# Performance work log

Hardware: AMD Instinct MI355X
Metric: run time of the kernel (lower is better)

Reference implementation:

```python
import jax, jax.numpy as jnp
import numpy as np

N, E, DIN, H, HEADS = 50000, 800000, 128, 64, 4


def setup_inputs() -> dict:
    key = jax.random.key(0)
    ks = jax.random.split(key, 12)

    def p(k, shape, fan_in):
        return jax.random.normal(k, shape, dtype=jnp.float32) / np.float32(np.sqrt(fan_in))

    return dict(
        x=jax.random.normal(ks[0], (N, DIN), dtype=jnp.float32),
        edge_index=jax.random.randint(ks[1], (2, E), 0, N, dtype=jnp.int32),
        # GCNConv(input_dim, hidden)
        W_gcn=p(ks[2], (DIN, H), DIN), b_gcn=jnp.zeros((H,), jnp.float32),
        # GATConv(hidden, hidden, heads=4, concat=True)
        W_gat=p(ks[3], (H, HEADS * H), H),
        att_src=p(ks[4], (HEADS, H), H), att_dst=p(ks[5], (HEADS, H), H),
        b_gat=jnp.zeros((HEADS * H,), jnp.float32),
        # SAGEConv(4*hidden, hidden): lin_l (neighbors, with bias), lin_r (root, no bias)
        W_sage_l=p(ks[6], (HEADS * H, H), HEADS * H), b_sage=jnp.zeros((H,), jnp.float32),
        W_sage_r=p(ks[7], (HEADS * H, H), HEADS * H),
        # edge-pair MLP: Linear(2*hidden, hidden) -> ReLU -> Linear(hidden, 1)
        W1=p(ks[8], (2 * H, H), 2 * H), b1=jnp.zeros((H,), jnp.float32),
        W2=p(ks[9], (H, 1), H), b2=jnp.zeros((1,), jnp.float32),
    )


def reference(x, edge_index, W_gcn, b_gcn, W_gat, att_src, att_dst, b_gat,
              W_sage_l, b_sage, W_sage_r, W1, b1, W2, b2):
    n = x.shape[0]
    src, dst = edge_index[0], edge_index[1]
    loop = jnp.arange(n, dtype=edge_index.dtype)
    # edges with self-loops appended (GCN and GAT add self-loops by default)
    s2 = jnp.concatenate([src, loop])
    d2 = jnp.concatenate([dst, loop])

    h = x @ W_gcn                                            # [N, H]
    deg = jax.ops.segment_sum(jnp.ones_like(d2, jnp.float32), d2, num_segments=n)
    dinv = jnp.where(deg > 0, jax.lax.rsqrt(jnp.maximum(deg, 1e-12)), 0.0)
    norm = dinv[s2] * dinv[d2]                               # [E+N]
    h = jax.ops.segment_sum(h[s2] * norm[:, None], d2, num_segments=n) + b_gcn
    h = jax.nn.relu(h)                                       # dropout: identity in eval

    # ---- GATConv (heads=4, concat=True, negative_slope=0.2) ----
    g = (h @ W_gat).reshape(n, HEADS, H)                     # [N, heads, C]
    a_s = jnp.sum(g * att_src, axis=-1)                      # [N, heads]
    a_d = jnp.sum(g * att_dst, axis=-1)
    e = jax.nn.leaky_relu(a_s[s2] + a_d[d2], 0.2)            # [E+N, heads]
    m = jax.ops.segment_max(e, d2, num_segments=n)           # per-target max (stable softmax)
    e = jnp.exp(e - m[d2])
    z = jax.ops.segment_sum(e, d2, num_segments=n)
    alpha = e / (z[d2] + 1e-16)                              # edge softmax over incoming edges
    g = jax.ops.segment_sum(g[s2] * alpha[:, :, None], d2, num_segments=n)
    g = jax.nn.relu(g.reshape(n, HEADS * H) + b_gat)

    # ---- SAGEConv (mean aggregation, root weight, no self-loops) ----
    nsum = jax.ops.segment_sum(g[src], dst, num_segments=n)
    cnt = jax.ops.segment_sum(jnp.ones_like(dst, jnp.float32), dst, num_segments=n)
    mean = nsum / jnp.maximum(cnt, 1.0)[:, None]
    s = jax.nn.relu(mean @ W_sage_l + b_sage + g @ W_sage_r)  # [N, H]

    # ---- edge-pair MLP + sigmoid ----
    ef = jnp.concatenate([s[src], s[dst]], axis=1)            # [E, 2H]
    pred = jax.nn.relu(ef @ W1 + b1) @ W2 + b2                # [E, 1]
    return jax.nn.sigmoid(pred[:, 0])
```

## Files before the change

### kernel.cpp

```cpp
#include <hip/hip_runtime.h>
#include <math.h>

typedef float v2f __attribute__((ext_vector_type(2)));
static __device__ __forceinline__ float4 f4s(float v){ return make_float4(v,v,v,v); }
static __device__ __forceinline__ float4 f4add(float4 a, float4 b){ return make_float4(a.x+b.x,a.y+b.y,a.z+b.z,a.w+b.w); }
static __device__ __forceinline__ float4 f4max(float4 a, float4 b){ return make_float4(fmaxf(a.x,b.x),fmaxf(a.y,b.y),fmaxf(a.z,b.z),fmaxf(a.w,b.w)); }
static __device__ __forceinline__ float4 f4scale(float4 a, float s){ return make_float4(a.x*s,a.y*s,a.z*s,a.w*s); }
static __device__ __forceinline__ float4 f4fma(float4 acc, float s, float4 b){
  acc.x += s*b.x; acc.y += s*b.y; acc.z += s*b.z; acc.w += s*b.w; return acc;
}
static __device__ __forceinline__ float4 f4relu(float4 a){ return f4max(a, f4s(0.f)); }
static __device__ __forceinline__ float4 f4leaky(float4 a){
  return make_float4(a.x>0.f?a.x:0.2f*a.x, a.y>0.f?a.y:0.2f*a.y, a.z>0.f?a.z:0.2f*a.z, a.w>0.f?a.w:0.2f*a.w);
}
static __device__ __forceinline__ float4 f4expf(float4 a){ return make_float4(__expf(a.x),__expf(a.y),__expf(a.z),__expf(a.w)); }
static __device__ __forceinline__ unsigned short f2bf(float f){
  unsigned int u = __float_as_uint(f);
  unsigned int r = (u + 0x7fffu + ((u >> 16) & 1u)) >> 16;
  return (unsigned short)r;
}
static __device__ __forceinline__ ushort4 f2bf4(float4 f){
  ushort4 r; r.x=f2bf(f.x); r.y=f2bf(f.y); r.z=f2bf(f.z); r.w=f2bf(f.w); return r;
}
static __device__ __forceinline__ float4 bfu2f4(uint2 u){
  return make_float4(__uint_as_float(u.x << 16), __uint_as_float(u.x & 0xffff0000u),
                     __uint_as_float(u.y << 16), __uint_as_float(u.y & 0xffff0000u));
}
static __device__ __forceinline__ float4 bfu2f4_lo(uint4 u){ return bfu2f4(make_uint2(u.x, u.y)); }
static __device__ __forceinline__ float4 bfu2f4_hi(uint4 u){ return bfu2f4(make_uint2(u.z, u.w)); }

typedef __attribute__((ext_vector_type(8))) unsigned short u16x8;
static __device__ __forceinline__ u16x8 f2bf8(float4 a, float4 b){
  u16x8 r;
  r[0]=f2bf(a.x); r[1]=f2bf(a.y); r[2]=f2bf(a.z); r[3]=f2bf(a.w);
  r[4]=f2bf(b.x); r[5]=f2bf(b.y); r[6]=f2bf(b.z); r[7]=f2bf(b.w);
  return r;
}
static __device__ __forceinline__ void red2(float4& a, float4& b){
  a.x += __shfl_xor(a.x, 8); a.y += __shfl_xor(a.y, 8);
  a.z += __shfl_xor(a.z, 8); a.w += __shfl_xor(a.w, 8);
  b.x += __shfl_xor(b.x, 8); b.y += __shfl_xor(b.y, 8);
  b.z += __shfl_xor(b.z, 8); b.w += __shfl_xor(b.w, 8);
}
static __device__ __forceinline__ unsigned char f2fp8(float v){
  return (unsigned char)(__builtin_amdgcn_cvt_pk_fp8_f32(v, v, 0, false) & 0xff);
}
static __device__ __forceinline__ unsigned int f4_fp8x4(float4 v){
  unsigned int r = __builtin_amdgcn_cvt_pk_fp8_f32(v.x, v.y, 0, false);
  r = __builtin_amdgcn_cvt_pk_fp8_f32(v.z, v.w, r, true);
  return r;
}
static __device__ __forceinline__ float4 fp8x4_f4(unsigned int q){
  v2f lo = __builtin_amdgcn_cvt_pk_f32_fp8(q, false);
  v2f hi = __builtin_amdgcn_cvt_pk_f32_fp8(q, true);
  return make_float4(lo[0], lo[1], hi[0], hi[1]);
}
static __device__ __forceinline__ float dot8(float4 a, float4 b, const float* v){
  return a.x*v[0]+a.y*v[1]+a.z*v[2]+a.w*v[3]+b.x*v[4]+b.y*v[5]+b.z*v[6]+b.w*v[7];
}

typedef __attribute__((ext_vector_type(8))) short bf16x8;
typedef __attribute__((ext_vector_type(4))) float f32x4;

__global__ __launch_bounds__(256) void k_rank(const int* __restrict__ dst, int* __restrict__ cnt,
                                              int* __restrict__ rank, int E){
  int t = blockIdx.x*256 + threadIdx.x;
  if (t < E) rank[t] = atomicAdd(&cnt[dst[t]], 1);
}
__global__ __launch_bounds__(256) void k_scan1(const int* __restrict__ cnt, int* __restrict__ excl,
                                               int* __restrict__ bsum, int n){
  __shared__ int sc[256];
  int t = threadIdx.x; int i = blockIdx.x*256 + t;
  int v = (i<n)?cnt[i]:0;
  sc[t]=v; __syncthreads();
  for (int o=1;o<256;o<<=1){ int a=(t>=o)?sc[t-o]:0; __syncthreads(); sc[t]+=a; __syncthreads(); }
  if (i<n) excl[i] = sc[t]-v;
  if (t==255) bsum[blockIdx.x] = sc[t];
}
__global__ __launch_bounds__(256) void k_scan2v(int* __restrict__ bsum, int nb,
                                                const float* __restrict__ Wg, const float* __restrict__ as,
                                                const float* __restrict__ ad, float* __restrict__ Vs,
                                                float* __restrict__ Vd){
  __shared__ int sc[256];
  int t = threadIdx.x;
  int v = (t<nb)?bsum[t]:0;
  sc[t]=v; __syncthreads();
  for (int o=1;o<256;o<<=1){ int a=(t>=o)?sc[t-o]:0; __syncthreads(); sc[t]+=a; __syncthreads(); }
  if (t<nb) bsum[t] = sc[t]-v;
  int h = t >> 6, k = t & 63;
  float s = 0.f, d = 0.f;
  const float* wr = Wg + (size_t)k*256 + h*64;
  const float* ar = as + h*64;
  const float* dr = ad + h*64;
  for (int c = 0; c < 64; ++c){ float w = wr[c]; s += w*ar[c]; d += w*dr[c]; }
  Vs[t] = s; Vd[t] = d;
}
__global__ __launch_bounds__(256) void k_scan3(const int* __restrict__ cnt, const int* __restrict__ excl,
                                               const int* __restrict__ bsum, int* __restrict__ offs,
                                               float* __restrict__ dinv, int n, int E){
  int i = blockIdx.x*256 + threadIdx.x;
  if (i < n){
    int o = excl[i] + bsum[blockIdx.x];
    offs[i] = o;
    dinv[i] = rsqrtf((float)cnt[i] + 1.0f);
    if (i == 0) offs[n] = E;
  }
}
__global__ __launch_bounds__(256) void k_fill(const int* __restrict__ src, const int* __restrict__ dst,
                                              const int* __restrict__ offs, const int* __restrict__ rank,
                                              int* __restrict__ csr, int E){
  int t = blockIdx.x*256 + threadIdx.x;
  if (t < E) csr[offs[dst[t]] + rank[t]] = src[t];
}

template<int K, int Cout, bool IBF16, bool SCALE, bool DUAL, bool H4, bool BRELU, bool OB16, bool O8>
__global__ __launch_bounds__(256) void k_mgemm(const void* __restrict__ in, int ldin,
                                               const float* __restrict__ Wa, int ldwa,
                                               const float* __restrict__ Wb, int ldwb,
                                               unsigned short* __restrict__ out,
                                               unsigned char* __restrict__ out8, int ldout,
                                               int n, const float* __restrict__ rowscale,
                                               const float* __restrict__ bias){
  constexpr int CC = Cout >> 4;
  constexpr int KB = K >> 5;
  constexpr int NH = H4 ? 4 : 1;
  extern __shared__ unsigned short wb[];
  int tid = threadIdx.x;
  constexpr int nslots = KB*CC*64;
  for (int s = tid; s < nslots; s += 256){
    int l = s & 63;
    int f = s >> 6;
    int cc = f % CC, kb = f / CC;
    int c  = cc*16 + (l & 15);
    int kr = kb*32 + ((l >> 4) << 3);
    const float* wp; int ld;
    if (DUAL && c >= (Cout/2)){ wp = Wb + (size_t)kr*ldwb + (c - Cout/2); ld = ldwb; }
    else                      { wp = Wa + (size_t)kr*ldwa + c;            ld = ldwa; }
    unsigned short* dp = &wb[s*8];
    #pragma unroll
    for (int j = 0; j < 8; ++j) dp[j] = f2bf(wp[(size_t)j*ld]);
  }
  __syncthreads();
  int wv = tid >> 6, l = tid & 63;
  int lrow = l & 15;
  int lk = (l >> 4) << 3;
  int ngrp = (n + 63) >> 6;
  const unsigned short* inb = (const unsigned short*)in;
  const float* inf = (const float*)in;
  for (int g = blockIdx.x; g < ngrp; g += gridDim.x){
    int r0 = (g << 6) + (wv << 4);
    int m = r0 + lrow;
    bf16x8 afr[NH][KB];
    #pragma unroll
    for (int h = 0; h < NH; ++h){
      #pragma unroll
      for (int kb = 0; kb < KB; ++kb){
        bf16x8 a = {0,0,0,0,0,0,0,0};
        if (m < n){
          int off = (H4 ? h*64 : 0) + kb*32 + lk;
          if (IBF16){
            a = *(const bf16x8*)(inb + (size_t)m*ldin + off);
          } else {
            const float* p = inf + (size_t)m*ldin + off;
            float4 f0 = *(const float4*)p;
            float4 f1 = *(const float4*)(p + 4);
            a[0]=(short)f2bf(f0.x); a[1]=(short)f2bf(f0.y); a[2]=(short)f2bf(f0.z); a[3]=(short)f2bf(f0.w);
            a[4]=(short)f2bf(f1.x); a[5]=(short)f2bf(f1.y); a[6]=(short)f2bf(f1.z); a[7]=(short)f2bf(f1.w);
          }
        }
        afr[h][kb] = a;
      }
    }
    int rbase = r0 + ((l >> 4) << 2);
    float sc[4];
    if (SCALE){
      #pragma unroll
      for (int r = 0; r < 4; ++r) sc[r] = (rbase + r < n) ? rowscale[rbase + r] : 0.f;
    }
    #pragma unroll
    for (int cc = 0; cc < CC; ++cc){
      f32x4 acc = {0.f, 0.f, 0.f, 0.f};
      constexpr int hstep = H4 ? 1 : 0;
      int hh = hstep ? (cc >> 2) : 0;
      #pragma unroll
      for (int kb = 0; kb < KB; ++kb){
        bf16x8 b = *(const bf16x8*)&wb[((kb*CC + cc)*64 + l)*8];
        acc = __builtin_amdgcn_mfma_f32_16x16x32_bf16(afr[hh][kb], b, acc, 0, 0, 0);
      }
      int c = cc*16 + lrow;
      float bv = BRELU ? bias[c] : 0.f;
      #pragma unroll
      for (int r = 0; r < 4; ++r){
        int rr = rbase + r;
        if (rr < n){
          float v = acc[r];
          if (SCALE) v *= sc[r];
          if (BRELU) v = fmaxf(v + bv, 0.f);
          if (OB16) out[(size_t)rr*ldout + c] = f2bf(v);
          if (O8)   out8[(size_t)rr*ldout + c] = f2fp8(v);
        }
      }
    }
  }
}

__global__ __launch_bounds__(256) void k_gatsage(const unsigned short* __restrict__ Y,
                                                 const float* __restrict__ Wg,
                                                 const float* __restrict__ bg,
                                                 const float* __restrict__ Wl,
                                                 const float* __restrict__ Wr,
                                                 unsigned short* __restrict__ R,
                                                 unsigned char* __restrict__ P8, int n){
  constexpr int LDG = 264;
  extern __shared__ unsigned short lds[];
  unsigned short* wb1 = lds;
  unsigned short* wb2 = wb1 + 2048*8;
  unsigned short* gb  = wb2 + 4096*8;
  int tid = threadIdx.x;
  for (int s = tid; s < 2048; s += 256){
    int l = s & 63, f = s >> 6;
    int cc = f & 15, kb = f >> 4;
    int c  = cc*16 + (l & 15);
    int kr = kb*32 + ((l >> 4) << 3);
    const float* wp = Wg + (size_t)kr*256 + c;
    unsigned short* dp = &wb1[s*8];
    #pragma unroll
    for (int j = 0; j < 8; ++j) dp[j] = f2bf(wp[(size_t)j*256]);
  }
  for (int s = tid; s < 4096; s += 256){
    int l = s & 63, f = s >> 6;
    int cc = f & 7, kb = f >> 3;
    int c  = cc*16 + (l & 15);
    int kr = kb*32 + ((l >> 4) << 3);
    const float* wp = (c >= 64) ? (Wr + (size_t)kr*64 + (c - 64)) : (Wl + (size_t)kr*64 + c);
    unsigned short* dp = &wb2[s*8];
    #pragma unroll
    for (int j = 0; j < 8; ++j) dp[j] = f2bf(wp[(size_t)j*64]);
  }
  __syncthreads();
  int wv = tid >> 6, l = tid & 63;
  int lrow = l & 15;
  int lk = (l >> 4) << 3;
  int rbase4 = (l >> 4) << 2;
  int ngrp = (n + 63) >> 6;
  for (int g = blockIdx.x; g < ngrp; g += gridDim.x){
    int r0 = (g << 6) + (wv << 4);
    int m = r0 + lrow;
    bf16x8 afr[4][2];
    #pragma unroll
    for (int h = 0; h < 4; ++h){
      #pragma unroll
      for (int kb = 0; kb < 2; ++kb){
        bf16x8 a = {0,0,0,0,0,0,0,0};
        if (m < n) a = *(const bf16x8*)(Y + (size_t)m*256 + h*64 + kb*32 + lk);
        afr[h][kb] = a;
      }
    }
    #pragma unroll
    for (int cc = 0; cc < 16; ++cc){
      f32x4 acc = {0.f, 0.f, 0.f, 0.f};
      int hh = cc >> 2;
      #pragma unroll
      for (int kb = 0; kb < 2; ++kb){
        bf16x8 b = *(const bf16x8*)&wb1[((kb*16 + cc)*64 + l)*8];
        acc = __builtin_amdgcn_mfma_f32_16x16x32_bf16(afr[hh][kb], b, acc, 0, 0, 0);
      }
      int c = cc*16 + lrow;
      float bv = bg[c];
      #pragma unroll
      for (int r = 0; r < 4; ++r){
        int lr = (wv << 4) + rbase4 + r;
        gb[lr*LDG + c] = f2bf(fmaxf(acc[r] + bv, 0.f));
      }
    }
    bf16x8 afb[8];
    #pragma unroll
    for (int kb = 0; kb < 8; ++kb)
      afb[kb] = *(const bf16x8*)&gb[((wv << 4) + lrow)*LDG + kb*32 + lk];
    #pragma unroll
    for (int cc = 0; cc < 8; ++cc){
      f32x4 acc = {0.f, 0.f, 0.f, 0.f};
      #pragma unroll
      for (int kb = 0; kb < 8; ++kb){
        bf16x8 b = *(const bf16x8*)&wb2[((kb*8 + cc)*64 + l)*8];
        acc = __builtin_amdgcn_mfma_f32_16x16x32_bf16(afb[kb], b, acc, 0, 0, 0);
      }
      int c = cc*16 + lrow;
      #pragma unroll
      for (int r = 0; r < 4; ++r){
        int rr = r0 + rbase4 + r;
        if (rr < n){
          float v = acc[r];
          if (c < 64) P8[(size_t)rr*64 + c] = f2fp8(v);
          else        R[(size_t)rr*64 + (c - 64)] = f2bf(v);
        }
      }
    }
  }
}

__global__ __launch_bounds__(256) void k_gcn(const unsigned char* __restrict__ a8, const float* __restrict__ dinv,
                                             const float* __restrict__ b, const int* __restrict__ offs,
                                             const int* __restrict__ csr, const float* __restrict__ Vs,
                                             const float* __restrict__ Vd, unsigned char* __restrict__ h8,
                                             float* __restrict__ D, int n){
  __shared__ float svs[256], svd[256];
  svs[threadIdx.x] = Vs[threadIdx.x];
  svd[threadIdx.x] = Vd[threadIdx.x];
  __syncthreads();
  int l = threadIdx.x & 63;
  int node = (((blockIdx.x*256 + threadIdx.x) >> 6) << 2) + (l >> 4);
  int l15 = l & 15;
  int grp = l15 >> 3, sub = l15 & 7;
  bool ok = node < n;
  int beg = 0, end = 0;
  float di = 0.f;
  if (ok){ beg = offs[node]; end = offs[node+1]; di = dinv[node]; }
  float4 aL0 = f4s(0.f), aH0 = f4s(0.f), aL1 = f4s(0.f), aH1 = f4s(0.f);
  int i = beg + grp;
  for (; i + 2 < end; i += 4){
    int s0 = csr[i], s1 = csr[i+2];
    uint2 u0 = *(const uint2*)(a8 + (size_t)s0*64 + (sub<<3));
    uint2 u1 = *(const uint2*)(a8 + (size_t)s1*64 + (sub<<3));
    aL0 = f4add(aL0, fp8x4_f4(u0.x)); aH0 = f4add(aH0, fp8x4_f4(u0.y));
    aL1 = f4add(aL1, fp8x4_f4(u1.x)); aH1 = f4add(aH1, fp8x4_f4(u1.y));
  }
  if (i < end){
    int s0 = csr[i];
    uint2 u0 = *(const uint2*)(a8 + (size_t)s0*64 + (sub<<3));
    aL0 = f4add(aL0, fp8x4_f4(u0.x)); aH0 = f4add(aH0, fp8x4_f4(u0.y));
  }
  float4 aL = f4add(aL0, aL1), aH = f4add(aH0, aH1);
  red2(aL, aH);
  if (ok){
    uint2 us = *(const uint2*)(a8 + (size_t)node*64 + (sub<<3));
    aL = f4add(aL, fp8x4_f4(us.x)); aH = f4add(aH, fp8x4_f4(us.y));
    float4 b0 = *(const float4*)(b + (sub<<3));
    float4 b1 = *(const float4*)(b + (sub<<3) + 4);
    float4 r0 = f4relu(f4fma(b0, di, aL));
    float4 r1 = f4relu(f4fma(b1, di, aH));
    if (grp == 0){
      uint2 q; q.x = f4_fp8x4(r0); q.y = f4_fp8x4(r1);
      *(uint2*)(h8 + (size_t)node*64 + (sub<<3)) = q;
    }
    const float* vs0 = svs + (grp*128) + (sub<<3);
    const float* vd0 = svd + (grp*128) + (sub<<3);
    float s0 = dot8(r0, r1, vs0);
    float s1 = dot8(r0, r1, vs0 + 64);
    float d0 = dot8(r0, r1, vd0);
    float d1 = dot8(r0, r1, vd0 + 64);
    #pragma unroll
    for (int o = 1; o < 8; o <<= 1){
      s0 += __shfl_xor(s0, o); s1 += __shfl_xor(s1, o);
      d0 += __shfl_xor(d0, o); d1 += __shfl_xor(d1, o);
    }
    if (sub == 0){
      *(float2*)(D + (size_t)node*8 + grp*2)     = make_float2(s0, s1);
      *(float2*)(D + (size_t)node*8 + 4 + grp*2) = make_float2(d0, d1);
    }
  }
}

#define GAT_CAP 128
__global__ __launch_bounds__(256) void k_gat2(const float* __restrict__ D, const unsigned char* __restrict__ H8,
                                              const int* __restrict__ offs, const int* __restrict__ csr,
                                              unsigned short* __restrict__ Y, int n){
  __shared__ float wl[8][GAT_CAP*4];
  __shared__ int   sl[8][GAT_CAP];
  int hw = threadIdx.x >> 5;
  int node = (blockIdx.x*256 + threadIdx.x) >> 5;
  int l5 = threadIdx.x & 31;
  if (node >= n) return;
  int beg = offs[node], end = offs[node+1];
  int deg = end - beg;
  float4 ed  = *(const float4*)(D + (size_t)node*8 + 4);
  float4 es0 = *(const float4*)(D + (size_t)node*8);
  float4 wself = f4expf(f4leaky(f4add(es0, ed)));
  float4 z4 = f4s(0.f);
  for (int i = beg + l5; i < end; i += 32){
    int s = csr[i];
    float4 w = f4expf(f4leaky(f4add(*(const float4*)(D + (size_t)s*8), ed)));
    int li = i - beg;
    if (li < GAT_CAP){ *(float4*)&wl[hw][li<<2] = w; sl[hw][li] = s << 6; }
    z4 = f4add(z4, w);
  }
  for (int m = 1; m < 32; m <<= 1){
    z4.x += __shfl_xor(z4.x, m); z4.y += __shfl_xor(z4.y, m);
    z4.z += __shfl_xor(z4.z, m); z4.w += __shfl_xor(z4.w, m);
  }
  z4 = f4add(z4, wself);
  int grp = l5 >> 4;
  int sub = l5 & 15;
  int c0b = sub << 2;
  float4 a0 = f4s(0.f), a1 = f4s(0.f), a2 = f4s(0.f), a3 = f4s(0.f);
  int nl = deg < GAT_CAP ? deg : GAT_CAP;
  int i = grp;
  for (; i + 2 < nl; i += 4){
    int o0 = sl[hw][i], o1 = sl[hw][i+2];
    float4 w0 = *(const float4*)&wl[hw][i<<2];
    float4 w1 = *(const float4*)&wl[hw][(i+2)<<2];
    unsigned int q0 = *(const unsigned int*)(H8 + o0 + c0b);
    unsigned int q1 = *(const unsigned int*)(H8 + o1 + c0b);
    float4 f0 = fp8x4_f4(q0);
    float4 f1 = fp8x4_f4(q1);
    a0 = f4fma(a0, w0.x, f0); a1 = f4fma(a1, w0.y, f0);
    a2 = f4fma(a2, w0.z, f0); a3 = f4fma(a3, w0.w, f0);
    a0 = f4fma(a0, w1.x, f1); a1 = f4fma(a1, w1.y, f1);
    a2 = f4fma(a2, w1.z, f1); a3 = f4fma(a3, w1.w, f1);
  }
  if (i < nl){
    float4 w0 = *(const float4*)&wl[hw][i<<2];
    float4 f0 = fp8x4_f4(*(const unsigned int*)(H8 + sl[hw][i] + c0b));
    a0 = f4fma(a0, w0.x, f0); a1 = f4fma(a1, w0.y, f0);
    a2 = f4fma(a2, w0.z, f0); a3 = f4fma(a3, w0.w, f0);
  }
  for (int j = nl + grp; j < deg; j += 2){
    int s = csr[beg+j];
    float4 e = f4leaky(f4add(*(const float4*)(D + (size_t)s*8), ed));
    float4 w = f4expf(e);
    float4 f0 = fp8x4_f4(*(const unsigned int*)(H8 + ((size_t)s << 6) + c0b));
    a0 = f4fma(a0, w.x, f0); a1 = f4fma(a1, w.y, f0);
    a2 = f4fma(a2, w.z, f0); a3 = f4fma(a3, w.w, f0);
  }
  a0.x += __shfl_xor(a0.x, 16); a0.y += __shfl_xor(a0.y, 16); a0.z += __shfl_xor(a0.z, 16); a0.w += __shfl_xor(a0.w, 16);
  a1.x += __shfl_xor(a1.x, 16); a1.y += __shfl_xor(a1.y, 16); a1.z += __shfl_xor(a1.z, 16); a1.w += __shfl_xor(a1.w, 16);
  a2.x += __shfl_xor(a2.x, 16); a2.y += __shfl_xor(a2.y, 16); a2.z += __shfl_xor(a2.z, 16); a2.w += __shfl_xor(a2.w, 16);
  a3.x += __shfl_xor(a3.x, 16); a3.y += __shfl_xor(a3.y, 16); a3.z += __shfl_xor(a3.z, 16); a3.w += __shfl_xor(a3.w, 16);
  if (grp == 0){
    float4 fs = fp8x4_f4(*(const unsigned int*)(H8 + ((size_t)node << 6) + c0b));
    a0 = f4fma(a0, wself.x, fs);
    a1 = f4fma(a1, wself.y, fs);
    a2 = f4fma(a2, wself.z, fs);
    a3 = f4fma(a3, wself.w, fs);
    a0 = f4scale(a0, 1.f/(z4.x + 1e-16f));
    a1 = f4scale(a1, 1.f/(z4.y + 1e-16f));
    a2 = f4scale(a2, 1.f/(z4.z + 1e-16f));
    a3 = f4scale(a3, 1.f/(z4.w + 1e-16f));
    unsigned short* yp = Y + (size_t)node*256 + (sub << 2);
    *(ushort4*)(yp)       = f2bf4(a0);
    *(ushort4*)(yp + 64)  = f2bf4(a1);
    *(ushort4*)(yp + 128) = f2bf4(a2);
    *(ushort4*)(yp + 192) = f2bf4(a3);
  }
}

__global__ __launch_bounds__(256) void k_sage(const unsigned char* __restrict__ P8, const unsigned short* __restrict__ R,
                                              const float* __restrict__ b, const int* __restrict__ offs,
                                              const int* __restrict__ csr, const float* __restrict__ W1a,
                                              const float* __restrict__ W1b, unsigned char* __restrict__ T2, int n){
  __shared__ unsigned short wfr[1024*8];
  __shared__ unsigned short stile[16][72];
  int tid = threadIdx.x;
  for (int s = tid; s < 1024; s += 256){
    int l = s & 63, f = s >> 6;
    int cc = f & 7, kb = f >> 3;
    int c  = cc*16 + (l & 15);
    int kr = kb*32 + ((l >> 4) << 3);
    const float* wp = (c >= 64) ? (W1b + (size_t)kr*64 + (c - 64)) : (W1a + (size_t)kr*64 + c);
    unsigned short* dp = &wfr[s*8];
    #pragma unroll
    for (int j = 0; j < 8; ++j) dp[j] = f2bf(wp[(size_t)j*64]);
  }
  int wv = tid >> 6, l = tid & 63;
  int base = blockIdx.x*16;
  int lrow16 = (wv << 2) + (l >> 4);
  int node = base + lrow16;
  int l15 = l & 15;
  int grp = l15 >> 3, sub = l15 & 7;
  bool ok = node < n;
  int beg = 0, end = 0;
  if (ok){ beg = offs[node]; end = offs[node+1]; }
  float4 aL0 = f4s(0.f), aH0 = f4s(0.f), aL1 = f4s(0.f), aH1 = f4s(0.f);
  int i = beg + grp;
  for (; i + 2 < end; i += 4){
    int s0 = csr[i], s1 = csr[i+2];
    uint2 u0 = *(const uint2*)(P8 + (size_t)s0*64 + (sub<<3));
    uint2 u1 = *(const uint2*)(P8 + (size_t)s1*64 + (sub<<3));
    aL0 = f4add(aL0, fp8x4_f4(u0.x)); aH0 = f4add(aH0, fp8x4_f4(u0.y));
    aL1 = f4add(aL1, fp8x4_f4(u1.x)); aH1 = f4add(aH1, fp8x4_f4(u1.y));
  }
  if (i < end){
    int s0 = csr[i];
    uint2 u0 = *(const uint2*)(P8 + (size_t)s0*64 + (sub<<3));
    aL0 = f4add(aL0, fp8x4_f4(u0.x)); aH0 = f4add(aH0, fp8x4_f4(u0.y));
  }
  float4 aL = f4add(aL0, aL1), aH = f4add(aH0, aH1);
  red2(aL, aH);
  float4 r0 = f4s(0.f), r1 = f4s(0.f);
  if (ok){
    float minv = 1.f / fmaxf((float)(end - beg), 1.f);
    uint4 ur = *(const uint4*)(R + (size_t)node*64 + (sub<<3));
    float4 b0 = *(const float4*)(b + (sub<<3));
    float4 b1 = *(const float4*)(b + (sub<<3) + 4);
    r0 = f4relu(f4add(f4fma(b0, minv, aL), bfu2f4_lo(ur)));
    r1 = f4relu(f4add(f4fma(b1, minv, aH), bfu2f4_hi(ur)));
  }
  if (grp == 0) *(u16x8*)&stile[lrow16][sub << 3] = f2bf8(r0, r1);
  __syncthreads();
  int lrow = l & 15, lk = (l >> 4) << 3;
  bf16x8 af0 = *(const bf16x8*)&stile[lrow][lk];
  bf16x8 af1 = *(const bf16x8*)&stile[lrow][32 + lk];
  int rbase = (l >> 4) << 2;
  #pragma unroll
  for (int q = 0; q < 2; ++q){
    int cc = wv*2 + q;
    f32x4 acc = {0.f, 0.f, 0.f, 0.f};
    acc = __builtin_amdgcn_mfma_f32_16x16x32_bf16(af0, *(const bf16x8*)&wfr[(cc*64 + l)*8], acc, 0, 0, 0);
    acc = __builtin_amdgcn_mfma_f32_16x16x32_bf16(af1, *(const bf16x8*)&wfr[((8 + cc)*64 + l)*8], acc, 0, 0, 0);
    int c = cc*16 + lrow;
    #pragma unroll
    for (int r = 0; r < 4; ++r){
      int nd = base + rbase + r;
      if (nd < n) T2[(size_t)nd*128 + c] = f2fp8(acc[r]);
    }
  }
}

__global__ __launch_bounds__(256) void k_mlp(const unsigned char* __restrict__ T2,
                                             const float* __restrict__ b1, const float* __restrict__ W2,
                                             const float* __restrict__ b2, const int* __restrict__ src,
                                             const int* __restrict__ dst, float* __restrict__ out, int E){
  int t = threadIdx.x;
  int e = blockIdx.x*32 + (t >> 3);
  if (e >= E) return;
  int sub = t & 7;
  int s = src[e], d = dst[e];
  uint2 uu = *(const uint2*)(T2 + (size_t)s*128 + (sub<<3));
  uint2 vv = *(const uint2*)(T2 + (size_t)d*128 + 64 + (sub<<3));
  float4 u0 = fp8x4_f4(uu.x), u1 = fp8x4_f4(uu.y);
  float4 v0 = fp8x4_f4(vv.x), v1 = fp8x4_f4(vv.y);
  float4 bb0 = *(const float4*)(b1 + (sub<<3));
  float4 bb1 = *(const float4*)(b1 + (sub<<3) + 4);
  float4 w0 = *(const float4*)(W2 + (sub<<3));
  float4 w1 = *(const float4*)(W2 + (sub<<3) + 4);
  float4 ta = f4relu(f4add(f4add(u0, v0), bb0));
  float4 tb = f4relu(f4add(f4add(u1, v1), bb1));
  float p = ta.x*w0.x + ta.y*w0.y + ta.z*w0.z + ta.w*w0.w
          + tb.x*w1.x + tb.y*w1.y + tb.z*w1.z + tb.w*w1.w;
  p += __shfl_xor(p, 1);
  p += __shfl_xor(p, 2);
  p += __shfl_xor(p, 4);
  if (sub == 0) out[e] = 1.f / (1.f + __expf(-(p + b2[0])));
}

extern "C" void kernel_launch(void* const* d_in, const int* in_sizes, int n_in,
                              void* d_out, int out_size, void* d_ws, size_t ws_size,
                              hipStream_t stream){
  const float* x     = (const float*)d_in[0];
  const int*   eidx  = (const int*)  d_in[1];
  const float* W_gcn = (const float*)d_in[2];
  const float* b_gcn = (const float*)d_in[3];
  const float* W_gat = (const float*)d_in[4];
  const float* att_s = (const float*)d_in[5];
  const float* att_d = (const float*)d_in[6];
  const float* b_gat = (const float*)d_in[7];
  const float* W_sl  = (const float*)d_in[8];
  const float* b_sg  = (const float*)d_in[9];
  const float* W_sr  = (const float*)d_in[10];
  const float* W1    = (const float*)d_in[11];
  const float* b1    = (const float*)d_in[12];
  const float* W2    = (const float*)d_in[13];
  const float* b2    = (const float*)d_in[14];
  float* out = (float*)d_out;

  const int N = in_sizes[0] / 128;
  const int E = in_sizes[1] / 2;
  const int* src = eidx;
  const int* dst = eidx + E;

  float* ws   = (float*)d_ws;
  float* dinv = ws;
  float* D    = dinv + (size_t)N;
  float* Vs   = D + (size_t)N*8;
  float* Vd   = Vs + 256;
  unsigned short* Y  = (unsigned short*)(Vd + 256);
  unsigned short* R  = Y + (size_t)N*256;
  unsigned char*  A8 = (unsigned char*)(R + (size_t)N*64);
  unsigned char*  H8 = A8 + (size_t)N*64;
  unsigned char*  P8 = H8 + (size_t)N*64;
  unsigned char*  T2 = P8 + (size_t)N*64;
  int* cnt  = (int*)(T2 + (size_t)N*128);
  int* excl = cnt + N;
  int* bsum = excl + N;
  int* offs = bsum + 256;
  int* rank = offs + N + 1;
  int* csr  = rank + E;

  const int nb = (N + 255) / 256;
  const int gtiles = (N + 63) / 64;
  const int nwb = (N + 15) / 16;
  const int GSH = (2048*8 + 4096*8 + 64*264) * 2;

  static bool s_attr = false;
  if (!s_attr){
    hipFuncSetAttribute((const void*)k_gatsage, hipFuncAttributeMaxDynamicSharedMemorySize, GSH);
    s_attr = true;
  }

  hipMemsetAsync(cnt, 0, (size_t)N*sizeof(int), stream);
  k_rank<<<(E+255)/256, 256, 0, stream>>>(dst, cnt, rank, E);
  k_scan1<<<nb, 256, 0, stream>>>(cnt, excl, bsum, N);
  k_scan2v<<<1, 256, 0, stream>>>(bsum, nb, W_gat, att_s, att_d, Vs, Vd);
  k_scan3<<<nb, 256, 0, stream>>>(cnt, excl, bsum, offs, dinv, N, E);
  k_fill<<<(E+255)/256, 256, 0, stream>>>(src, dst, offs, rank, csr, E);

  k_mgemm<128, 64, false, true, false, false, false, false, true><<<gtiles, 256, 128*64*2, stream>>>(
      x, 128, W_gcn, 64, nullptr, 0, nullptr, A8, 64, N, dinv, nullptr);
  k_gcn <<<nwb, 256, 0, stream>>>(A8, dinv, b_gcn, offs, csr, Vs, Vd, H8, D, N);

  k_gat2<<<(N+7)/8, 256, 0, stream>>>(D, H8, offs, csr, Y, N);

  k_gatsage<<<256, 256, GSH, stream>>>(Y, W_gat, b_gat, W_sl, W_sr, R, P8, N);

  k_sage<<<nwb, 256, 0, stream>>>(P8, R, b_sg, offs, csr, W1, W1 + 64*64, T2, N);

  k_mlp <<<(E+31)/32, 256, 0, stream>>>(T2, b1, W2, b2, src, dst, out, E);
}
```

Before: 290.5 us.

## Merge preprocessing kernels to cut launches: fold scan2 into scan1/scan3, fuse fill with GCN GEMM

Moves the attention-vector precomputation into an extra block of the first scan kernel. Each block of the third scan now redoes the block-sum scan itself, which removes the single-block second scan launch. The CSR fill and the GCN input GEMM (x·W_gcn scaled by dinv, written as fp8) share one launch, with block ranges assigned to each job. This cuts the launch count from seven to four and lets the GEMM overlap the irregular scatter, at the cost of redundant block-sum scans and a specialized, non-persistent GEMM.

New measurement: 285.6 us. Within noise of the previous version (-1.7%).

```diff
diff --git a/kernel.cpp b/kernel.cpp
--- a/kernel.cpp
+++ b/kernel.cpp
@@ -67,8 +67,22 @@
   int t = blockIdx.x*256 + threadIdx.x;
   if (t < E) rank[t] = atomicAdd(&cnt[dst[t]], 1);
 }
-__global__ __launch_bounds__(256) void k_scan1(const int* __restrict__ cnt, int* __restrict__ excl,
-                                               int* __restrict__ bsum, int n){
+__global__ __launch_bounds__(256) void k_scan1v(const int* __restrict__ cnt, int* __restrict__ excl,
+                                                int* __restrict__ bsum, int n, int nb,
+                                                const float* __restrict__ Wg, const float* __restrict__ as,
+                                                const float* __restrict__ ad, float* __restrict__ Vs,
+                                                float* __restrict__ Vd){
+  if ((int)blockIdx.x == nb){
+    int t = threadIdx.x;
+    int h = t >> 6, k = t & 63;
+    float s = 0.f, d = 0.f;
+    const float* wr = Wg + (size_t)k*256 + h*64;
+    const float* ar = as + h*64;
+    const float* dr = ad + h*64;
+    for (int c = 0; c < 64; ++c){ float w = wr[c]; s += w*ar[c]; d += w*dr[c]; }
+    Vs[t] = s; Vd[t] = d;
+    return;
+  }
   __shared__ int sc[256];
   int t = threadIdx.x; int i = blockIdx.x*256 + t;
   int v = (i<n)?cnt[i]:0;
@@ -77,129 +91,83 @@
   if (i<n) excl[i] = sc[t]-v;
   if (t==255) bsum[blockIdx.x] = sc[t];
 }
-__global__ __launch_bounds__(256) void k_scan2v(int* __restrict__ bsum, int nb,
-                                                const float* __restrict__ Wg, const float* __restrict__ as,
-                                                const float* __restrict__ ad, float* __restrict__ Vs,
-                                                float* __restrict__ Vd){
-  __shared__ int sc[256];
+__global__ __launch_bounds__(256) void k_scan3b(const int* __restrict__ cnt, const int* __restrict__ excl,
+                                                const int* __restrict__ bsum, int* __restrict__ offs,
+                                                float* __restrict__ dinv, int n, int E, int nb){
+  __shared__ int sb[256];
   int t = threadIdx.x;
   int v = (t<nb)?bsum[t]:0;
-  sc[t]=v; __syncthreads();
-  for (int o=1;o<256;o<<=1){ int a=(t>=o)?sc[t-o]:0; __syncthreads(); sc[t]+=a; __syncthreads(); }
-  if (t<nb) bsum[t] = sc[t]-v;
-  int h = t >> 6, k = t & 63;
-  float s = 0.f, d = 0.f;
-  const float* wr = Wg + (size_t)k*256 + h*64;
-  const float* ar = as + h*64;
-  const float* dr = ad + h*64;
-  for (int c = 0; c < 64; ++c){ float w = wr[c]; s += w*ar[c]; d += w*dr[c]; }
-  Vs[t] = s; Vd[t] = d;
-}
-__global__ __launch_bounds__(256) void k_scan3(const int* __restrict__ cnt, const int* __restrict__ excl,
-                                               const int* __restrict__ bsum, int* __restrict__ offs,
-                                               float* __restrict__ dinv, int n, int E){
-  int i = blockIdx.x*256 + threadIdx.x;
+  sb[t]=v; __syncthreads();
+  for (int o=1;o<256;o<<=1){ int a=(t>=o)?sb[t-o]:0; __syncthreads(); sb[t]+=a; __syncthreads(); }
+  int bex = sb[blockIdx.x] - bsum[blockIdx.x];
+  int i = blockIdx.x*256 + t;
   if (i < n){
-    int o = excl[i] + bsum[blockIdx.x];
-    offs[i] = o;
+    offs[i] = excl[i] + bex;
     dinv[i] = rsqrtf((float)cnt[i] + 1.0f);
     if (i == 0) offs[n] = E;
   }
 }
-__global__ __launch_bounds__(256) void k_fill(const int* __restrict__ src, const int* __restrict__ dst,
-                                              const int* __restrict__ offs, const int* __restrict__ rank,
-                                              int* __restrict__ csr, int E){
-  int t = blockIdx.x*256 + threadIdx.x;
-  if (t < E) csr[offs[dst[t]] + rank[t]] = src[t];
-}
-
-template<int K, int Cout, bool IBF16, bool SCALE, bool DUAL, bool H4, bool BRELU, bool OB16, bool O8>
-__global__ __launch_bounds__(256) void k_mgemm(const void* __restrict__ in, int ldin,
-                                               const float* __restrict__ Wa, int ldwa,
-                                               const float* __restrict__ Wb, int ldwb,
-                                               unsigned short* __restrict__ out,
-                                               unsigned char* __restrict__ out8, int ldout,
-                                               int n, const float* __restrict__ rowscale,
-                                               const float* __restrict__ bias){
-  constexpr int CC = Cout >> 4;
-  constexpr int KB = K >> 5;
-  constexpr int NH = H4 ? 4 : 1;
-  extern __shared__ unsigned short wb[];
+
+__global__ __launch_bounds__(256) void k_fillg(const int* __restrict__ src, const int* __restrict__ dstv,
+                                               const int* __restrict__ offs, const int* __restrict__ rank,
+                                               int* __restrict__ csr, int E, int fb,
+                                               const float* __restrict__ x, const float* __restrict__ Wg,
+                                               unsigned char* __restrict__ a8, int n,
+                                               const float* __restrict__ dinv){
+  if ((int)blockIdx.x < fb){
+    int t = blockIdx.x*256 + threadIdx.x;
+    if (t < E) csr[offs[dstv[t]] + rank[t]] = src[t];
+    return;
+  }
+  __shared__ unsigned short wb[1024*8];
   int tid = threadIdx.x;
-  constexpr int nslots = KB*CC*64;
-  for (int s = tid; s < nslots; s += 256){
-    int l = s & 63;
-    int f = s >> 6;
-    int cc = f % CC, kb = f / CC;
+  for (int s = tid; s < 1024; s += 256){
+    int l = s & 63, f = s >> 6;
+    int cc = f & 3, kb = f >> 2;
     int c  = cc*16 + (l & 15);
     int kr = kb*32 + ((l >> 4) << 3);
-    const float* wp; int ld;
-    if (DUAL && c >= (Cout/2)){ wp = Wb + (size_t)kr*ldwb + (c - Cout/2); ld = ldwb; }
-    else                      { wp = Wa + (size_t)kr*ldwa + c;            ld = ldwa; }
+    const float* wp = Wg + (size_t)kr*64 + c;
     unsigned short* dp = &wb[s*8];
     #pragma unroll
-    for (int j = 0; j < 8; ++j) dp[j] = f2bf(wp[(size_t)j*ld]);
+    for (int j = 0; j < 8; ++j) dp[j] = f2bf(wp[(size_t)j*64]);
   }
   __syncthreads();
   int wv = tid >> 6, l = tid & 63;
   int lrow = l & 15;
   int lk = (l >> 4) << 3;
-  int ngrp = (n + 63) >> 6;
-  const unsigned short* inb = (const unsigned short*)in;
-  const float* inf = (const float*)in;
-  for (int g = blockIdx.x; g < ngrp; g += gridDim.x){
-    int r0 = (g << 6) + (wv << 4);
-    int m = r0 + lrow;
-    bf16x8 afr[NH][KB];
-    #pragma unroll
-    for (int h = 0; h < NH; ++h){
-      #pragma unroll
-      for (int kb = 0; kb < KB; ++kb){
-        bf16x8 a = {0,0,0,0,0,0,0,0};
-        if (m < n){
-          int off = (H4 ? h*64 : 0) + kb*32 + lk;
-          if (IBF16){
-            a = *(const bf16x8*)(inb + (size_t)m*ldin + off);
-          } else {
-            const float* p = inf + (size_t)m*ldin + off;
-            float4 f0 = *(const float4*)p;
-            float4 f1 = *(const float4*)(p + 4);
-            a[0]=(short)f2bf(f0.x); a[1]=(short)f2bf(f0.y); a[2]=(short)f2bf(f0.z); a[3]=(short)f2bf(f0.w);
-            a[4]=(short)f2bf(f1.x); a[5]=(short)f2bf(f1.y); a[6]=(short)f2bf(f1.z); a[7]=(short)f2bf(f1.w);
-          }
-        }
-        afr[h][kb] = a;
-      }
-    }
-    int rbase = r0 + ((l >> 4) << 2);
-    float sc[4];
-    if (SCALE){
-      #pragma unroll
-      for (int r = 0; r < 4; ++r) sc[r] = (rbase + r < n) ? rowscale[rbase + r] : 0.f;
-    }
-    #pragma unroll
-    for (int cc = 0; cc < CC; ++cc){
-      f32x4 acc = {0.f, 0.f, 0.f, 0.f};
-      constexpr int hstep = H4 ? 1 : 0;
-      int hh = hstep ? (cc >> 2) : 0;
-      #pragma unroll
-      for (int kb = 0; kb < KB; ++kb){
-        bf16x8 b = *(const bf16x8*)&wb[((kb*CC + cc)*64 + l)*8];
-        acc = __builtin_amdgcn_mfma_f32_16x16x32_bf16(afr[hh][kb], b, acc, 0, 0, 0);
-      }
-      int c = cc*16 + lrow;
-      float bv = BRELU ? bias[c] : 0.f;
-      #pragma unroll
-      for (int r = 0; r < 4; ++r){
-        int rr = rbase + r;
-        if (rr < n){
-          float v = acc[r];
-          if (SCALE) v *= sc[r];
-          if (BRELU) v = fmaxf(v + bv, 0.f);
-          if (OB16) out[(size_t)rr*ldout + c] = f2bf(v);
-          if (O8)   out8[(size_t)rr*ldout + c] = f2fp8(v);
-        }
-      }
+  int g = blockIdx.x - fb;
+  int r0 = (g << 6) + (wv << 4);
+  int m = r0 + lrow;
+  bf16x8 afr[4];
+  #pragma unroll
+  for (int kb = 0; kb < 4; ++kb){
+    bf16x8 a = {0,0,0,0,0,0,0,0};
+    if (m < n){
+      const float* p = x + (size_t)m*128 + kb*32 + lk;
+      float4 f0 = *(const float4*)p;
+      float4 f1 = *(const float4*)(p + 4);
+      a[0]=(short)f2bf(f0.x); a[1]=(short)f2bf(f0.y); a[2]=(short)f2bf(f0.z); a[3]=(short)f2bf(f0.w);
+      a[4]=(short)f2bf(f1.x); a[5]=(short)f2bf(f1.y); a[6]=(short)f2bf(f1.z); a[7]=(short)f2bf(f1.w);
+    }
+    afr[kb] = a;
+  }
+  int rbase = r0 + ((l >> 4) << 2);
+  float sc[4];
+  #pragma unroll
+  for (int r = 0; r < 4; ++r) sc[r] = (rbase + r < n) ? dinv[rbase + r] : 0.f;
+  #pragma unroll
+  for (int cc = 0; cc < 4; ++cc){
+    f32x4 acc = {0.f, 0.f, 0.f, 0.f};
+    #pragma unroll
+    for (int kb = 0; kb < 4; ++kb){
+      bf16x8 b = *(const bf16x8*)&wb[((kb*4 + cc)*64 + l)*8];
+      acc = __builtin_amdgcn_mfma_f32_16x16x32_bf16(afr[kb], b, acc, 0, 0, 0);
+    }
+    int c = cc*16 + lrow;
+    #pragma unroll
+    for (int r = 0; r < 4; ++r){
+      int rr = rbase + r;
+      if (rr < n) a8[(size_t)rr*64 + c] = f2fp8(acc[r] * sc[r]);
     }
   }
 }
@@ -587,6 +555,7 @@
   int* csr  = rank + E;
 
   const int nb = (N + 255) / 256;
+  const int fb = (E + 255) / 256;
   const int gtiles = (N + 63) / 64;
   const int nwb = (N + 15) / 16;
   const int GSH = (2048*8 + 4096*8 + 64*264) * 2;
@@ -598,14 +567,12 @@
   }
 
   hipMemsetAsync(cnt, 0, (size_t)N*sizeof(int), stream);
-  k_rank<<<(E+255)/256, 256, 0, stream>>>(dst, cnt, rank, E);
-  k_scan1<<<nb, 256, 0, stream>>>(cnt, excl, bsum, N);
-  k_scan2v<<<1, 256, 0, stream>>>(bsum, nb, W_gat, att_s, att_d, Vs, Vd);
-  k_scan3<<<nb, 256, 0, stream>>>(cnt, excl, bsum, offs, dinv, N, E);
-  k_fill<<<(E+255)/256, 256, 0, stream>>>(src, dst, offs, rank, csr, E);
-
-  k_mgemm<128, 64, false, true, false, false, false, false, true><<<gtiles, 256, 128*64*2, stream>>>(
-      x, 128, W_gcn, 64, nullptr, 0, nullptr, A8, 64, N, dinv, nullptr);
+  k_rank  <<<fb, 256, 0, stream>>>(dst, cnt, rank, E);
+  k_scan1v<<<nb + 1, 256, 0, stream>>>(cnt, excl, bsum, N, nb, W_gat, att_s, att_d, Vs, Vd);
+  k_scan3b<<<nb, 256, 0, stream>>>(cnt, excl, bsum, offs, dinv, N, E, nb);
+  k_fillg <<<fb + gtiles, 256, 0, stream>>>(src, dst, offs, rank, csr, E, fb,
+                                            x, W_gcn, A8, N, dinv);
+
   k_gcn <<<nwb, 256, 0, stream>>>(A8, dinv, b_gcn, offs, csr, Vs, Vd, H8, D, N);
 
   k_gat2<<<(N+7)/8, 256, 0, stream>>>(D, H8, offs, csr, Y, N);
```
